# Optimization experiments

Measured on AMD Instinct MI355X. Metric: run time of the kernel, lower is better.

## Reference

```python
import jax, jax.numpy as jnp
import numpy as np

B, D, H, E, TOPK = 8192, 1024, 4096, 8, 2


def setup_inputs() -> dict:
    key = jax.random.key(0)
    ks = jax.random.split(key, 5)
    s_in = 1.0 / np.sqrt(D)
    s_h = 1.0 / np.sqrt(H)
    return {
        "x": jax.random.normal(ks[0], (B, D), jnp.float32),
        "Wg": jax.random.normal(ks[1], (D, E), jnp.float32) * s_in,
        "bg": jnp.zeros((E,), jnp.float32),
        "W1": jax.random.normal(ks[2], (E, D, H), jnp.float32) * s_in,
        "b1": jnp.zeros((E, H), jnp.float32),
        "W2": jax.random.normal(ks[3], (E, H, D), jnp.float32) * s_h,
        "b2": jnp.zeros((E, D), jnp.float32),
    }


def reference(x, Wg, bg, W1, b1, W2, b2):
    # Gating: softmax over experts, top-k, renormalize selected weights
    logits = x @ Wg + bg                              # [B, E]
    weights = jax.nn.softmax(logits, axis=-1)
    topw, topi = jax.lax.top_k(weights, TOPK)         # [B, k]
    topw = topw / jnp.sum(topw, axis=-1, keepdims=True)
    # Dense combine weights: [B, E], zero for unselected experts
    comb = jnp.sum(topw[..., None] * jax.nn.one_hot(topi, E, dtype=x.dtype), axis=1)
    # Expert MLPs computed batched per expert (grouped GEMM form)
    h = jax.nn.gelu(jnp.einsum('bd,edh->ebh', x, W1) + b1[:, None, :], approximate=False)  # [E,B,H]
    y = jnp.einsum('ebh,ehd->ebd', h, W2) + b2[:, None, :]                                 # [E,B,D]
    # Weighted combine: only top-k experts have nonzero weight
    out = jnp.einsum('ebd,be->bd', y, comb)           # [B, D]
    return out
```

## Files before the change

### kernel.cpp

```cpp
#include <hip/hip_runtime.h>
#include <stdint.h>

#define B_TOK 8192
#define DDIM 1024
#define HDIM 4096
#define NEXP 8

typedef __bf16 bf16x8 __attribute__((ext_vector_type(8)));
typedef float f32x4 __attribute__((ext_vector_type(4)));

__device__ __forceinline__ unsigned short f2bf(float f) {
  unsigned int u = __float_as_uint(f);
  u += 0x7fffu + ((u >> 16) & 1u);
  return (unsigned short)(u >> 16);
}
__device__ __forceinline__ float bfhi(unsigned int u) {
  return __uint_as_float(u & 0xffff0000u);
}
__device__ __forceinline__ float bflo(unsigned int u) {
  return __uint_as_float(u << 16);
}

__device__ __forceinline__ void gld16(const void* g, void* l) {
  __builtin_amdgcn_global_load_lds(
      (const __attribute__((address_space(1))) void*)g,
      (__attribute__((address_space(3))) void*)l, 16, 0, 0);
}

__device__ __forceinline__ float gelu_f(float v) {
  float u = v * (0.7978845608f + 0.0356774081f * v * v);
  float ex = __expf(2.f * u);
  float th = 1.f - 2.f * __builtin_amdgcn_rcpf(ex + 1.f);
  return 0.5f * v * (1.f + th);
}

__global__ __launch_bounds__(256) void gating_kernel(
    const float* __restrict__ x, const float* __restrict__ Wg,
    const float* __restrict__ bg, int* __restrict__ t2e,
    float* __restrict__ t2w, int* __restrict__ cnt) {
  __shared__ float sWg[NEXP * DDIM];
  int tid = threadIdx.x;
  for (int i = tid; i < NEXP * DDIM; i += 256) {
    int d = i >> 3, e = i & 7;
    sWg[e * DDIM + d] = Wg[i];
  }
  __syncthreads();
  int lane = tid & 63, wave = tid >> 6;
  for (int t = 0; t < 16; ++t) {
    int b = blockIdx.x * 64 + wave * 16 + t;
    float acc[NEXP];
#pragma unroll
    for (int e = 0; e < NEXP; ++e) acc[e] = 0.f;
    const float* xr = x + (size_t)b * DDIM;
#pragma unroll
    for (int j = 0; j < 4; ++j) {
      int d0 = j * 256 + lane * 4;
      float4 xv = *(const float4*)(xr + d0);
#pragma unroll
      for (int e = 0; e < NEXP; ++e) {
        float4 wv = *(const float4*)(sWg + e * DDIM + d0);
        acc[e] += xv.x * wv.x + xv.y * wv.y + xv.z * wv.z + xv.w * wv.w;
      }
    }
#pragma unroll
    for (int off = 32; off > 0; off >>= 1) {
#pragma unroll
      for (int e = 0; e < NEXP; ++e) acc[e] += __shfl_xor(acc[e], off);
    }
    if (lane == 0) {
      float l0[NEXP];
#pragma unroll
      for (int e = 0; e < NEXP; ++e) l0[e] = acc[e] + bg[e];
      int i1 = 0;
      float v1 = l0[0];
#pragma unroll
      for (int e = 1; e < NEXP; ++e)
        if (l0[e] > v1) { v1 = l0[e]; i1 = e; }
      int i2 = (i1 == 0) ? 1 : 0;
      float v2 = l0[i2];
#pragma unroll
      for (int e = 0; e < NEXP; ++e)
        if (e != i1 && l0[e] > v2) { v2 = l0[e]; i2 = e; }
      float w1 = 1.f / (1.f + expf(v2 - v1));
      float w2 = 1.f - w1;
      t2e[b * 2] = i1;
      t2e[b * 2 + 1] = i2;
      t2w[b * 2] = w1;
      t2w[b * 2 + 1] = w2;
      atomicAdd(&cnt[i1], 1);
      atomicAdd(&cnt[i2], 1);
    }
  }
}

__global__ void prefix_kernel(const int* __restrict__ cnt, int* __restrict__ offs,
                              int* __restrict__ tileE, int* __restrict__ tileM,
                              int* __restrict__ ntile) {
  int s = 0, t = 0;
  offs[0] = 0;
  for (int e = 0; e < NEXP; ++e) {
    int c = cnt[e];
    for (int m = 0; m < c; m += 128) { tileE[t] = e; tileM[t] = m; ++t; }
    s += c;
    offs[e + 1] = s;
  }
  *ntile = t;
}

__global__ __launch_bounds__(256) void scatter_kernel(
    const int* __restrict__ t2e, const int* __restrict__ offs,
    int* __restrict__ cursor, int* __restrict__ tok, int* __restrict__ rowpos) {
  int b = blockIdx.x * 256 + threadIdx.x;
  if (b >= B_TOK) return;
#pragma unroll
  for (int k = 0; k < 2; ++k) {
    int e = t2e[b * 2 + k];
    int pos = offs[e] + atomicAdd(&cursor[e], 1);
    tok[pos] = b;
    rowpos[b * 2 + k] = pos;
  }
}

__global__ __launch_bounds__(256) void cvt_x_kernel(const float* __restrict__ x,
                                                    unsigned short* __restrict__ xb) {
  size_t i = ((size_t)blockIdx.x * 256 + threadIdx.x) * 4;
  float4 v = *(const float4*)(x + i);
  ushort4 o;
  o.x = f2bf(v.x);
  o.y = f2bf(v.y);
  o.z = f2bf(v.z);
  o.w = f2bf(v.w);
  *(ushort4*)(xb + i) = o;
}

__global__ __launch_bounds__(256) void transpose_cvt_kernel(
    const float* __restrict__ src, unsigned short* __restrict__ dst, int R, int C) {
  __shared__ unsigned short T[64][72];
  size_t eo = (size_t)blockIdx.z * (size_t)R * C;
  int c0 = blockIdx.x * 64, r0 = blockIdx.y * 64;
  int tid = threadIdx.x;
#pragma unroll
  for (int p = 0; p < 4; ++p) {
    int idx = p * 256 + tid;
    int r = idx >> 4, c4 = (idx & 15) * 4;
    float4 v = *(const float4*)(src + eo + (size_t)(r0 + r) * C + c0 + c4);
    T[r][c4] = f2bf(v.x);
    T[r][c4 + 1] = f2bf(v.y);
    T[r][c4 + 2] = f2bf(v.z);
    T[r][c4 + 3] = f2bf(v.w);
  }
  __syncthreads();
#pragma unroll
  for (int p = 0; p < 2; ++p) {
    int idx = p * 256 + tid;
    int c = idx >> 3, s8 = (idx & 7) * 8;
    ushort4 a, b;
    a.x = T[s8][c];     a.y = T[s8 + 1][c]; a.z = T[s8 + 2][c]; a.w = T[s8 + 3][c];
    b.x = T[s8 + 4][c]; b.y = T[s8 + 5][c]; b.z = T[s8 + 6][c]; b.w = T[s8 + 7][c];
    unsigned short* dp = dst + eo + (size_t)(c0 + c) * R + r0 + s8;
    *(ushort4*)dp = a;
    *(ushort4*)(dp + 4) = b;
  }
}

__global__ __launch_bounds__(256) void gemm1_kernel(
    const unsigned short* __restrict__ xb, const unsigned short* __restrict__ w1t,
    const float* __restrict__ b1, const int* __restrict__ offs,
    const int* __restrict__ tileE, const int* __restrict__ tileM,
    const int* __restrict__ ntile, const int* __restrict__ tok,
    unsigned short* __restrict__ hbuf) {
  int ty = blockIdx.y;
  if (ty >= *ntile) return;
  int e = tileE[ty], m0 = tileM[ty];
  int r0 = offs[e], rows = offs[e + 1] - r0;
  int n0 = blockIdx.x * 128;

  __shared__ __attribute__((aligned(16))) unsigned short Ws[128 * 32];
  __shared__ __attribute__((aligned(16))) unsigned short Xs[128 * 32];

  int tid = threadIdx.x, lane = tid & 63, wave = tid >> 6;
  int u0 = wave * 2, u1 = u0 + 1;
  int sr = lane >> 2, sk = (lane & 3) * 8;
  int nr0 = u0 * 16 + sr, nr1 = u1 * 16 + sr;
  const unsigned short* pW0 = w1t + ((size_t)e * HDIM + n0 + nr0) * DDIM + sk;
  const unsigned short* pW1 = w1t + ((size_t)e * HDIM + n0 + nr1) * DDIM + sk;
  int ma0 = min(m0 + nr0, rows - 1), ma1 = min(m0 + nr1, rows - 1);
  const unsigned short* pX0 = xb + (size_t)tok[r0 + ma0] * DDIM + sk;
  const unsigned short* pX1 = xb + (size_t)tok[r0 + ma1] * DDIM + sk;

  f32x4 acc[4][4];
#pragma unroll
  for (int i = 0; i < 4; ++i)
#pragma unroll
    for (int j = 0; j < 4; ++j) acc[i][j] = (f32x4){0.f, 0.f, 0.f, 0.f};

  int wn = wave & 1, wm = wave >> 1;
  int nbase = wn * 64, mbase = wm * 64;
  int fr = lane & 15, quad = lane >> 4;

  for (int kk = 0; kk < DDIM; kk += 32) {
    gld16(pW0 + kk, Ws + u0 * 512);
    gld16(pW1 + kk, Ws + u1 * 512);
    gld16(pX0 + kk, Xs + u0 * 512);
    gld16(pX1 + kk, Xs + u1 * 512);
    __syncthreads();
    bf16x8 a[4], b[4];
#pragma unroll
    for (int i = 0; i < 4; ++i) {
      a[i] = *(const bf16x8*)(Ws + (size_t)(nbase + i * 16 + fr) * 32 + quad * 8);
      b[i] = *(const bf16x8*)(Xs + (size_t)(mbase + i * 16 + fr) * 32 + quad * 8);
    }
#pragma unroll
    for (int i = 0; i < 4; ++i)
#pragma unroll
      for (int j = 0; j < 4; ++j)
        acc[i][j] = __builtin_amdgcn_mfma_f32_16x16x32_bf16(a[i], b[j], acc[i][j], 0, 0, 0);
    __syncthreads();
  }

  const float* b1e = b1 + (size_t)e * HDIM + n0 + nbase;
  float4 bias[4];
#pragma unroll
  for (int i = 0; i < 4; ++i) bias[i] = *(const float4*)(b1e + i * 16 + quad * 4);
#pragma unroll
  for (int j = 0; j < 4; ++j) {
    int grow = m0 + mbase + j * 16 + fr;
    if (grow < rows) {
      unsigned short* hp = hbuf + (size_t)(r0 + grow) * HDIM + n0 + nbase;
#pragma unroll
      for (int i = 0; i < 4; ++i) {
        ushort4 o;
        o.x = f2bf(gelu_f(acc[i][j][0] + bias[i].x));
        o.y = f2bf(gelu_f(acc[i][j][1] + bias[i].y));
        o.z = f2bf(gelu_f(acc[i][j][2] + bias[i].z));
        o.w = f2bf(gelu_f(acc[i][j][3] + bias[i].w));
        *(ushort4*)(hp + i * 16 + quad * 4) = o;
      }
    }
  }
}

__global__ __launch_bounds__(256) void gemm2_kernel(
    const unsigned short* __restrict__ hbuf, const unsigned short* __restrict__ w2t,
    const float* __restrict__ b2, const int* __restrict__ offs,
    const int* __restrict__ tileE, const int* __restrict__ tileM,
    const int* __restrict__ ntile, unsigned short* __restrict__ ybuf) {
  int ty = blockIdx.y;
  if (ty >= *ntile) return;
  int e = tileE[ty], m0 = tileM[ty];
  int r0 = offs[e], rows = offs[e + 1] - r0;
  int n0 = blockIdx.x * 128;

  __shared__ __attribute__((aligned(16))) unsigned short Ws[128 * 32];
  __shared__ __attribute__((aligned(16))) unsigned short Hs[128 * 32];

  int tid = threadIdx.x, lane = tid & 63, wave = tid >> 6;
  int u0 = wave * 2, u1 = u0 + 1;
  int sr = lane >> 2, sk = (lane & 3) * 8;
  int nr0 = u0 * 16 + sr, nr1 = u1 * 16 + sr;
  const unsigned short* pW0 = w2t + ((size_t)e * DDIM + n0 + nr0) * HDIM + sk;
  const unsigned short* pW1 = w2t + ((size_t)e * DDIM + n0 + nr1) * HDIM + sk;
  const unsigned short* pH0 = hbuf + (size_t)(r0 + min(m0 + nr0, rows - 1)) * HDIM + sk;
  const unsigned short* pH1 = hbuf + (size_t)(r0 + min(m0 + nr1, rows - 1)) * HDIM + sk;

  f32x4 acc[4][4];
#pragma unroll
  for (int i = 0; i < 4; ++i)
#pragma unroll
    for (int j = 0; j < 4; ++j) acc[i][j] = (f32x4){0.f, 0.f, 0.f, 0.f};

  int wn = wave & 1, wm = wave >> 1;
  int nbase = wn * 64, mbase = wm * 64;
  int fr = lane & 15, quad = lane >> 4;

  for (int kk = 0; kk < HDIM; kk += 32) {
    gld16(pW0 + kk, Ws + u0 * 512);
    gld16(pW1 + kk, Ws + u1 * 512);
    gld16(pH0 + kk, Hs + u0 * 512);
    gld16(pH1 + kk, Hs + u1 * 512);
    __syncthreads();
    bf16x8 a[4], b[4];
#pragma unroll
    for (int i = 0; i < 4; ++i) {
      a[i] = *(const bf16x8*)(Ws + (size_t)(nbase + i * 16 + fr) * 32 + quad * 8);
      b[i] = *(const bf16x8*)(Hs + (size_t)(mbase + i * 16 + fr) * 32 + quad * 8);
    }
#pragma unroll
    for (int i = 0; i < 4; ++i)
#pragma unroll
      for (int j = 0; j < 4; ++j)
        acc[i][j] = __builtin_amdgcn_mfma_f32_16x16x32_bf16(a[i], b[j], acc[i][j], 0, 0, 0);
    __syncthreads();
  }

  const float* b2e = b2 + (size_t)e * DDIM + n0 + nbase;
  float4 bias[4];
#pragma unroll
  for (int i = 0; i < 4; ++i) bias[i] = *(const float4*)(b2e + i * 16 + quad * 4);
#pragma unroll
  for (int j = 0; j < 4; ++j) {
    int grow = m0 + mbase + j * 16 + fr;
    if (grow < rows) {
      unsigned short* yp = ybuf + (size_t)(r0 + grow) * DDIM + n0 + nbase;
#pragma unroll
      for (int i = 0; i < 4; ++i) {
        ushort4 o;
        o.x = f2bf(acc[i][j][0] + bias[i].x);
        o.y = f2bf(acc[i][j][1] + bias[i].y);
        o.z = f2bf(acc[i][j][2] + bias[i].z);
        o.w = f2bf(acc[i][j][3] + bias[i].w);
        *(ushort4*)(yp + i * 16 + quad * 4) = o;
      }
    }
  }
}

__global__ __launch_bounds__(256) void combine_kernel(
    const unsigned short* __restrict__ ybuf, const int* __restrict__ rowpos,
    const float* __restrict__ t2w, float* __restrict__ out) {
  int idx = blockIdx.x * 256 + threadIdx.x;
  int b = idx >> 7;
  int c8 = (idx & 127) * 8;
  int p0 = rowpos[b * 2], p1 = rowpos[b * 2 + 1];
  float w0 = t2w[b * 2], w1 = t2w[b * 2 + 1];
  uint4 ya = *(const uint4*)(ybuf + (size_t)p0 * DDIM + c8);
  uint4 yb = *(const uint4*)(ybuf + (size_t)p1 * DDIM + c8);
  float4 o0, o1;
  o0.x = w0 * bflo(ya.x) + w1 * bflo(yb.x);
  o0.y = w0 * bfhi(ya.x) + w1 * bfhi(yb.x);
  o0.z = w0 * bflo(ya.y) + w1 * bflo(yb.y);
  o0.w = w0 * bfhi(ya.y) + w1 * bfhi(yb.y);
  o1.x = w0 * bflo(ya.z) + w1 * bflo(yb.z);
  o1.y = w0 * bfhi(ya.z) + w1 * bfhi(yb.z);
  o1.z = w0 * bflo(ya.w) + w1 * bflo(yb.w);
  o1.w = w0 * bfhi(ya.w) + w1 * bfhi(yb.w);
  float* op = out + (size_t)b * DDIM + c8;
  *(float4*)op = o0;
  *(float4*)(op + 4) = o1;
}

extern "C" void kernel_launch(void* const* d_in, const int* in_sizes, int n_in,
                              void* d_out, int out_size, void* d_ws, size_t ws_size,
                              hipStream_t stream) {
  const float* x = (const float*)d_in[0];
  const float* Wg = (const float*)d_in[1];
  const float* bg = (const float*)d_in[2];
  const float* W1 = (const float*)d_in[3];
  const float* b1 = (const float*)d_in[4];
  const float* W2 = (const float*)d_in[5];
  const float* b2 = (const float*)d_in[6];
  float* out = (float*)d_out;

  char* ws = (char*)d_ws;
  int* cnt = (int*)(ws + 0);
  int* cursor = (int*)(ws + 64);
  int* offs = (int*)(ws + 128);
  int* ntile = (int*)(ws + 192);
  int* tileE = (int*)(ws + 256);
  int* tileM = (int*)(ws + 896);
  int* t2e = (int*)(ws + 2048);
  float* t2w = (float*)(ws + 67584);
  int* tok = (int*)(ws + 133120);
  int* rowpos = (int*)(ws + 198656);
  char* big = ws + 264192;
  unsigned short* xb = (unsigned short*)big;
  unsigned short* w1t = (unsigned short*)(big + 16777216);
  unsigned short* ybuf = w1t;
  unsigned short* w2t = (unsigned short*)(big + 16777216 + 67108864);
  unsigned short* hbuf = (unsigned short*)(big + 16777216 + 2 * 67108864);

  (void)in_sizes; (void)n_in; (void)out_size; (void)ws_size;

  hipMemsetAsync(ws, 0, 256, stream);

  cvt_x_kernel<<<(B_TOK * DDIM) / 1024, 256, 0, stream>>>(x, xb);
  transpose_cvt_kernel<<<dim3(HDIM / 64, DDIM / 64, NEXP), 256, 0, stream>>>(W1, w1t, DDIM, HDIM);
  transpose_cvt_kernel<<<dim3(DDIM / 64, HDIM / 64, NEXP), 256, 0, stream>>>(W2, w2t, HDIM, DDIM);
  gating_kernel<<<B_TOK / 64, 256, 0, stream>>>(x, Wg, bg, t2e, t2w, cnt);
  prefix_kernel<<<1, 1, 0, stream>>>(cnt, offs, tileE, tileM, ntile);
  scatter_kernel<<<B_TOK / 256, 256, 0, stream>>>(t2e, offs, cursor, tok, rowpos);
  gemm1_kernel<<<dim3(HDIM / 128, 136), 256, 0, stream>>>(xb, w1t, b1, offs, tileE, tileM, ntile, tok, hbuf);
  gemm2_kernel<<<dim3(DDIM / 128, 136), 256, 0, stream>>>(hbuf, w2t, b2, offs, tileE, tileM, ntile, ybuf);
  combine_kernel<<<(B_TOK * DDIM) / (256 * 8), 256, 0, stream>>>(ybuf, rowpos, t2w, out);
}
```

Baseline: 1.054 ms.

## Replace expert GEMMs with 256x256 tiled, double-buffered, swizzled MFMA kernel

Merges the two grouped expert GEMMs into one templated kernel that uses 256x256 output tiles with 512 threads, a K-step of 64 split into two halves, and a double-buffered LDS pipeline driven by explicit vmcnt/lgkmcnt waits and raw barriers. LDS rows are XOR-swizzled to avoid bank conflicts, and MFMA sections are raised in priority with setprio. The routing tile size changes from 128 to 256 rows to match, which reduces the grid to MAXTILE=72 row tiles. The aim is to hide global-load latency and raise data reuse per tile. The cost is more LDS and registers per block and more padded rows for experts whose token counts are not multiples of 256.

```diff
diff --git a/kernel.cpp b/kernel.cpp
--- a/kernel.cpp
+++ b/kernel.cpp
@@ -5,6 +5,7 @@
 #define DDIM 1024
 #define HDIM 4096
 #define NEXP 8
+#define MAXTILE 72
 
 typedef __bf16 bf16x8 __attribute__((ext_vector_type(8)));
 typedef float f32x4 __attribute__((ext_vector_type(4)));
@@ -100,7 +101,7 @@
   offs[0] = 0;
   for (int e = 0; e < NEXP; ++e) {
     int c = cnt[e];
-    for (int m = 0; m < c; m += 128) { tileE[t] = e; tileM[t] = m; ++t; }
+    for (int m = 0; m < c; m += 256) { tileE[t] = e; tileM[t] = m; ++t; }
     s += c;
     offs[e + 1] = s;
   }
@@ -163,152 +164,188 @@
   }
 }
 
-__global__ __launch_bounds__(256) void gemm1_kernel(
-    const unsigned short* __restrict__ xb, const unsigned short* __restrict__ w1t,
-    const float* __restrict__ b1, const int* __restrict__ offs,
+#define BAR() __builtin_amdgcn_s_barrier()
+#define LG0() asm volatile("s_waitcnt lgkmcnt(0)" ::: "memory")
+#define VM6() asm volatile("s_waitcnt vmcnt(6)" ::: "memory")
+#define VM0() asm volatile("s_waitcnt vmcnt(0)" ::: "memory")
+#define RGN(t, mat, ks) (&LDS[(t) & 1][mat][ks][0][0])
+#define STAGE(mat, P0, P1, t, ks)                                   \
+  do {                                                              \
+    unsigned short* _d = RGN(t, mat, ks) + wave * 512;              \
+    gld16((P0) + (size_t)(t) * 64 + (ks) * 32, _d);                 \
+    gld16((P1) + (size_t)(t) * 64 + (ks) * 32, _d + 4096);          \
+  } while (0)
+#define RDA(t, ks)                                                  \
+  do {                                                              \
+    const unsigned short* _p = RGN(t, 0, ks);                       \
+    _Pragma("unroll") for (int n = 0; n < 4; ++n)                   \
+        a[n] = *(const bf16x8*)(_p + aoff[n]);                      \
+  } while (0)
+#define RDB(t, ks, h)                                               \
+  do {                                                              \
+    const unsigned short* _p = RGN(t, 1, ks);                       \
+    _Pragma("unroll") for (int m = 0; m < 4; ++m)                   \
+        b[m] = *(const bf16x8*)(_p + boff2[h][m]);                  \
+  } while (0)
+#define MMQ(h)                                                      \
+  do {                                                              \
+    __builtin_amdgcn_s_setprio(1);                                  \
+    _Pragma("unroll") for (int i = 0; i < 4; ++i)                   \
+        _Pragma("unroll") for (int j = 0; j < 4; ++j)               \
+            acc[i][(h)*4 + j] = __builtin_amdgcn_mfma_f32_16x16x32_bf16( \
+                a[i], b[j], acc[i][(h)*4 + j], 0, 0, 0);            \
+    __builtin_amdgcn_s_setprio(0);                                  \
+  } while (0)
+
+template <int KD, bool GELU, bool GATHER>
+__global__ __launch_bounds__(512, 2) void moe_gemm(
+    const unsigned short* __restrict__ Bsrc, const unsigned short* __restrict__ Wt,
+    const float* __restrict__ bias, const int* __restrict__ offs,
     const int* __restrict__ tileE, const int* __restrict__ tileM,
     const int* __restrict__ ntile, const int* __restrict__ tok,
-    unsigned short* __restrict__ hbuf) {
+    unsigned short* __restrict__ obuf, int ND) {
+  constexpr int NT = KD / 64;
+  __shared__ __attribute__((aligned(16))) unsigned short LDS[2][2][2][256][32];
   int ty = blockIdx.y;
   if (ty >= *ntile) return;
   int e = tileE[ty], m0 = tileM[ty];
   int r0 = offs[e], rows = offs[e + 1] - r0;
-  int n0 = blockIdx.x * 128;
-
-  __shared__ __attribute__((aligned(16))) unsigned short Ws[128 * 32];
-  __shared__ __attribute__((aligned(16))) unsigned short Xs[128 * 32];
-
+  int n0 = blockIdx.x * 256;
   int tid = threadIdx.x, lane = tid & 63, wave = tid >> 6;
-  int u0 = wave * 2, u1 = u0 + 1;
-  int sr = lane >> 2, sk = (lane & 3) * 8;
-  int nr0 = u0 * 16 + sr, nr1 = u1 * 16 + sr;
-  const unsigned short* pW0 = w1t + ((size_t)e * HDIM + n0 + nr0) * DDIM + sk;
-  const unsigned short* pW1 = w1t + ((size_t)e * HDIM + n0 + nr1) * DDIM + sk;
-  int ma0 = min(m0 + nr0, rows - 1), ma1 = min(m0 + nr1, rows - 1);
-  const unsigned short* pX0 = xb + (size_t)tok[r0 + ma0] * DDIM + sk;
-  const unsigned short* pX1 = xb + (size_t)tok[r0 + ma1] * DDIM + sk;
-
-  f32x4 acc[4][4];
+  int wn = wave & 3, wm = wave >> 2;
+  int nbase = wn * 64, mbase = wm * 128;
+  int fr = lane & 15, quad = lane >> 4;
+
+  int rs = tid >> 2;
+  int ss = (tid & 3) ^ ((rs >> 1) & 3);
+  const unsigned short* pA0 = Wt + ((size_t)e * ND + n0 + rs) * KD + ss * 8;
+  const unsigned short* pA1 = pA0 + (size_t)128 * KD;
+  int mr0 = min(m0 + rs, rows - 1), mr1 = min(m0 + 128 + rs, rows - 1);
+  size_t br0, br1;
+  if constexpr (GATHER) {
+    br0 = (size_t)tok[r0 + mr0];
+    br1 = (size_t)tok[r0 + mr1];
+  } else {
+    br0 = (size_t)(r0 + mr0);
+    br1 = (size_t)(r0 + mr1);
+  }
+  const unsigned short* pB0 = Bsrc + br0 * KD + ss * 8;
+  const unsigned short* pB1 = Bsrc + br1 * KD + ss * 8;
+
+  int aoff[4], boff2[2][4];
+#pragma unroll
+  for (int n = 0; n < 4; ++n) {
+    int rA = nbase + n * 16 + fr;
+    aoff[n] = rA * 32 + (quad ^ ((rA >> 1) & 3)) * 8;
+  }
+#pragma unroll
+  for (int h = 0; h < 2; ++h)
+#pragma unroll
+    for (int m = 0; m < 4; ++m) {
+      int rB = mbase + h * 64 + m * 16 + fr;
+      boff2[h][m] = rB * 32 + (quad ^ ((rB >> 1) & 3)) * 8;
+    }
+
+  f32x4 acc[4][8];
 #pragma unroll
   for (int i = 0; i < 4; ++i)
 #pragma unroll
-    for (int j = 0; j < 4; ++j) acc[i][j] = (f32x4){0.f, 0.f, 0.f, 0.f};
-
-  int wn = wave & 1, wm = wave >> 1;
-  int nbase = wn * 64, mbase = wm * 64;
-  int fr = lane & 15, quad = lane >> 4;
-
-  for (int kk = 0; kk < DDIM; kk += 32) {
-    gld16(pW0 + kk, Ws + u0 * 512);
-    gld16(pW1 + kk, Ws + u1 * 512);
-    gld16(pX0 + kk, Xs + u0 * 512);
-    gld16(pX1 + kk, Xs + u1 * 512);
-    __syncthreads();
-    bf16x8 a[4], b[4];
-#pragma unroll
-    for (int i = 0; i < 4; ++i) {
-      a[i] = *(const bf16x8*)(Ws + (size_t)(nbase + i * 16 + fr) * 32 + quad * 8);
-      b[i] = *(const bf16x8*)(Xs + (size_t)(mbase + i * 16 + fr) * 32 + quad * 8);
-    }
-#pragma unroll
-    for (int i = 0; i < 4; ++i)
-#pragma unroll
-      for (int j = 0; j < 4; ++j)
-        acc[i][j] = __builtin_amdgcn_mfma_f32_16x16x32_bf16(a[i], b[j], acc[i][j], 0, 0, 0);
-    __syncthreads();
-  }
-
-  const float* b1e = b1 + (size_t)e * HDIM + n0 + nbase;
-  float4 bias[4];
-#pragma unroll
-  for (int i = 0; i < 4; ++i) bias[i] = *(const float4*)(b1e + i * 16 + quad * 4);
-#pragma unroll
-  for (int j = 0; j < 4; ++j) {
-    int grow = m0 + mbase + j * 16 + fr;
+    for (int j = 0; j < 8; ++j) acc[i][j] = (f32x4){0.f, 0.f, 0.f, 0.f};
+  bf16x8 a[4], b[4];
+
+  STAGE(0, pA0, pA1, 0, 0);
+  STAGE(1, pB0, pB1, 0, 0);
+  STAGE(0, pA0, pA1, 0, 1);
+  STAGE(1, pB0, pB1, 0, 1);
+  STAGE(0, pA0, pA1, 1, 0);
+  STAGE(1, pB0, pB1, 1, 0);
+  STAGE(0, pA0, pA1, 1, 1);
+  VM6();
+  BAR();
+
+  for (int t = 0; t < NT - 2; ++t) {
+    RDA(t, 0); RDB(t, 0, 0);
+    STAGE(1, pB0, pB1, t + 1, 1);
+    BAR(); LG0();
+    MMQ(0);
+    BAR();
+    RDB(t, 0, 1);
+    STAGE(0, pA0, pA1, t + 2, 0);
+    BAR(); LG0();
+    MMQ(1);
+    BAR();
+    RDA(t, 1); RDB(t, 1, 0);
+    STAGE(1, pB0, pB1, t + 2, 0);
+    BAR(); LG0();
+    MMQ(0);
+    BAR();
+    RDB(t, 1, 1);
+    STAGE(0, pA0, pA1, t + 2, 1);
+    VM6();
+    BAR(); LG0();
+    MMQ(1);
+    BAR();
+  }
+  {
+    int t = NT - 2;
+    RDA(t, 0); RDB(t, 0, 0);
+    STAGE(1, pB0, pB1, t + 1, 1);
+    BAR(); LG0();
+    MMQ(0);
+    BAR();
+    RDB(t, 0, 1);
+    BAR(); LG0();
+    MMQ(1);
+    BAR();
+    RDA(t, 1); RDB(t, 1, 0);
+    BAR(); LG0();
+    MMQ(0);
+    BAR();
+    RDB(t, 1, 1);
+    VM0();
+    BAR(); LG0();
+    MMQ(1);
+    BAR();
+  }
+  {
+    int t = NT - 1;
+    RDA(t, 0); RDB(t, 0, 0);
+    BAR(); LG0();
+    MMQ(0);
+    BAR();
+    RDB(t, 0, 1);
+    BAR(); LG0();
+    MMQ(1);
+    BAR();
+    RDA(t, 1); RDB(t, 1, 0);
+    BAR(); LG0();
+    MMQ(0);
+    BAR();
+    RDB(t, 1, 1);
+    LG0();
+    MMQ(1);
+  }
+
+  const float* be = bias + (size_t)e * ND + n0 + nbase;
+  float4 bv[4];
+#pragma unroll
+  for (int i = 0; i < 4; ++i) bv[i] = *(const float4*)(be + i * 16 + quad * 4);
+#pragma unroll
+  for (int j = 0; j < 8; ++j) {
+    int grow = m0 + mbase + (j >> 2) * 64 + (j & 3) * 16 + fr;
     if (grow < rows) {
-      unsigned short* hp = hbuf + (size_t)(r0 + grow) * HDIM + n0 + nbase;
+      unsigned short* yp = obuf + (size_t)(r0 + grow) * ND + n0 + nbase;
 #pragma unroll
       for (int i = 0; i < 4; ++i) {
+        float v0 = acc[i][j][0] + bv[i].x;
+        float v1 = acc[i][j][1] + bv[i].y;
+        float v2 = acc[i][j][2] + bv[i].z;
+        float v3 = acc[i][j][3] + bv[i].w;
+        if constexpr (GELU) {
+          v0 = gelu_f(v0); v1 = gelu_f(v1); v2 = gelu_f(v2); v3 = gelu_f(v3);
+        }
         ushort4 o;
-        o.x = f2bf(gelu_f(acc[i][j][0] + bias[i].x));
-        o.y = f2bf(gelu_f(acc[i][j][1] + bias[i].y));
-        o.z = f2bf(gelu_f(acc[i][j][2] + bias[i].z));
-        o.w = f2bf(gelu_f(acc[i][j][3] + bias[i].w));
-        *(ushort4*)(hp + i * 16 + quad * 4) = o;
-      }
-    }
-  }
-}
-
-__global__ __launch_bounds__(256) void gemm2_kernel(
-    const unsigned short* __restrict__ hbuf, const unsigned short* __restrict__ w2t,
-    const float* __restrict__ b2, const int* __restrict__ offs,
-    const int* __restrict__ tileE, const int* __restrict__ tileM,
-    const int* __restrict__ ntile, unsigned short* __restrict__ ybuf) {
-  int ty = blockIdx.y;
-  if (ty >= *ntile) return;
-  int e = tileE[ty], m0 = tileM[ty];
-  int r0 = offs[e], rows = offs[e + 1] - r0;
-  int n0 = blockIdx.x * 128;
-
-  __shared__ __attribute__((aligned(16))) unsigned short Ws[128 * 32];
-  __shared__ __attribute__((aligned(16))) unsigned short Hs[128 * 32];
-
-  int tid = threadIdx.x, lane = tid & 63, wave = tid >> 6;
-  int u0 = wave * 2, u1 = u0 + 1;
-  int sr = lane >> 2, sk = (lane & 3) * 8;
-  int nr0 = u0 * 16 + sr, nr1 = u1 * 16 + sr;
-  const unsigned short* pW0 = w2t + ((size_t)e * DDIM + n0 + nr0) * HDIM + sk;
-  const unsigned short* pW1 = w2t + ((size_t)e * DDIM + n0 + nr1) * HDIM + sk;
-  const unsigned short* pH0 = hbuf + (size_t)(r0 + min(m0 + nr0, rows - 1)) * HDIM + sk;
-  const unsigned short* pH1 = hbuf + (size_t)(r0 + min(m0 + nr1, rows - 1)) * HDIM + sk;
-
-  f32x4 acc[4][4];
-#pragma unroll
-  for (int i = 0; i < 4; ++i)
-#pragma unroll
-    for (int j = 0; j < 4; ++j) acc[i][j] = (f32x4){0.f, 0.f, 0.f, 0.f};
-
-  int wn = wave & 1, wm = wave >> 1;
-  int nbase = wn * 64, mbase = wm * 64;
-  int fr = lane & 15, quad = lane >> 4;
-
-  for (int kk = 0; kk < HDIM; kk += 32) {
-    gld16(pW0 + kk, Ws + u0 * 512);
-    gld16(pW1 + kk, Ws + u1 * 512);
-    gld16(pH0 + kk, Hs + u0 * 512);
-    gld16(pH1 + kk, Hs + u1 * 512);
-    __syncthreads();
-    bf16x8 a[4], b[4];
-#pragma unroll
-    for (int i = 0; i < 4; ++i) {
-      a[i] = *(const bf16x8*)(Ws + (size_t)(nbase + i * 16 + fr) * 32 + quad * 8);
-      b[i] = *(const bf16x8*)(Hs + (size_t)(mbase + i * 16 + fr) * 32 + quad * 8);
-    }
-#pragma unroll
-    for (int i = 0; i < 4; ++i)
-#pragma unroll
-      for (int j = 0; j < 4; ++j)
-        acc[i][j] = __builtin_amdgcn_mfma_f32_16x16x32_bf16(a[i], b[j], acc[i][j], 0, 0, 0);
-    __syncthreads();
-  }
-
-  const float* b2e = b2 + (size_t)e * DDIM + n0 + nbase;
-  float4 bias[4];
-#pragma unroll
-  for (int i = 0; i < 4; ++i) bias[i] = *(const float4*)(b2e + i * 16 + quad * 4);
-#pragma unroll
-  for (int j = 0; j < 4; ++j) {
-    int grow = m0 + mbase + j * 16 + fr;
-    if (grow < rows) {
-      unsigned short* yp = ybuf + (size_t)(r0 + grow) * DDIM + n0 + nbase;
-#pragma unroll
-      for (int i = 0; i < 4; ++i) {
-        ushort4 o;
-        o.x = f2bf(acc[i][j][0] + bias[i].x);
-        o.y = f2bf(acc[i][j][1] + bias[i].y);
-        o.z = f2bf(acc[i][j][2] + bias[i].z);
-        o.w = f2bf(acc[i][j][3] + bias[i].w);
+        o.x = f2bf(v0); o.y = f2bf(v1); o.z = f2bf(v2); o.w = f2bf(v3);
         *(ushort4*)(yp + i * 16 + quad * 4) = o;
       }
     }
@@ -379,7 +416,9 @@
   gating_kernel<<<B_TOK / 64, 256, 0, stream>>>(x, Wg, bg, t2e, t2w, cnt);
   prefix_kernel<<<1, 1, 0, stream>>>(cnt, offs, tileE, tileM, ntile);
   scatter_kernel<<<B_TOK / 256, 256, 0, stream>>>(t2e, offs, cursor, tok, rowpos);
-  gemm1_kernel<<<dim3(HDIM / 128, 136), 256, 0, stream>>>(xb, w1t, b1, offs, tileE, tileM, ntile, tok, hbuf);
-  gemm2_kernel<<<dim3(DDIM / 128, 136), 256, 0, stream>>>(hbuf, w2t, b2, offs, tileE, tileM, ntile, ybuf);
+  moe_gemm<DDIM, true, true><<<dim3(HDIM / 256, MAXTILE), 512, 0, stream>>>(
+      xb, w1t, b1, offs, tileE, tileM, ntile, tok, hbuf, HDIM);
+  moe_gemm<HDIM, false, false><<<dim3(DDIM / 256, MAXTILE), 512, 0, stream>>>(
+      hbuf, w2t, b2, offs, tileE, tileM, ntile, tok, ybuf, DDIM);
   combine_kernel<<<(B_TOK * DDIM) / (256 * 8), 256, 0, stream>>>(ybuf, rowpos, t2w, out);
 }
```

Measured after the change: 993.6 us. 1.06x faster.
